# Optimization experiments

Measured on AMD Instinct MI355X. Metric: run time of the kernel, lower is better.

The kernel has to match this reference:

```python
import jax, jax.numpy as jnp
import numpy as np

N = 4096
K = 32
K_NEIGH = 5
LR_EDGE = 0.05
LR_GLOBAL_DECAY = 0.001
NOISE_STD = 0.05
RIPPLE_STRENGTH = 0.01
SPARK_ENERGY_DECAY = 0.98
SPARK_FORCE_STEPS = 5
SPARK_MIN_ENERGY = 0.05
STATE_DECAY = 0.95


def setup_inputs() -> dict:
    key = jax.random.key(0)
    k1, k2, k3 = jax.random.split(key, 3)
    return {
        "W": 0.1 * jax.random.normal(k1, (N, N), jnp.float32),
        "s": jnp.zeros((N,), jnp.float32),
        "noise": jax.random.normal(k2, (N,), jnp.float32),
        "spark_energy": jnp.ones((K,), jnp.float32),
        "u": jax.random.uniform(k3, (K,), jnp.float32),
        "spark_pos": jnp.arange(K, dtype=jnp.int32) % N,
        "spark_age": jnp.zeros((K,), jnp.int32),
    }


def _step(W, s, noise, spark_energy, u, spark_pos, spark_age):
    n = W.shape[0]
    k = spark_pos.shape[0]
    # state diffusion: decay, noisy matvec, sigmoid
    s = s * STATE_DECAY
    s = jax.nn.sigmoid(W @ s + NOISE_STD * noise)
    # force young sparks' positions to 1.0 (drop-mode scatter for masked writes)
    force_idx = jnp.where(spark_age < SPARK_FORCE_STEPS, spark_pos, n)
    s = s.at[force_idx].set(1.0, mode="drop")

    def body(carry, xs):
        W, s = carry
        i, prev, energy, age, ui = xs
        # multinomial over relu(W[prev]) via inverse-CDF on cumsum
        row = W[prev]
        w = jax.nn.relu(row) + 1e-6
        cdf = jnp.cumsum(w)
        nxt = jnp.minimum(
            jnp.searchsorted(cdf, ui * cdf[-1], side="right"), n - 1
        ).astype(prev.dtype)
        # edge learning on traversed edge
        W = W.at[nxt, prev].set(W[nxt, prev] * (1.0 - LR_EDGE) + s[prev] * LR_EDGE)
        # ripple to top-K neighbors of prev (row re-read AFTER edge update, as in torch)
        top = jax.lax.top_k(jax.nn.relu(W[prev]), K_NEIGH)[1]
        W = W.at[prev, top].add(RIPPLE_STRENGTH)
        W = W.at[top, prev].add(RIPPLE_STRENGTH * 0.5)
        W = W.at[top[:, None], top[None, :]].add(RIPPLE_STRENGTH * 0.3)
        # energy decay, deposit energy at new position
        energy = energy * SPARK_ENERGY_DECAY
        s = s.at[nxt].set(energy)
        age = age + 1
        # respawn exhausted sparks
        respawn = energy < SPARK_MIN_ENERGY
        pos_new = jnp.where(respawn, (i % n).astype(prev.dtype), nxt)
        energy = jnp.where(respawn, jnp.float32(1.0), energy)
        age = jnp.where(respawn, jnp.int32(0), age)
        return (W, s), (pos_new, energy, age)

    idx = jnp.arange(k, dtype=jnp.int32)
    (W, s), (pos, energy, age) = jax.lax.scan(
        body, (W, s), (idx, spark_pos, spark_energy, spark_age, u)
    )
    # global decay + clamp
    W = jnp.clip(W * (1.0 - LR_GLOBAL_DECAY), -2.0, 2.0)
    return s, W, pos, energy, age


def reference(W, s, noise, spark_energy, u, spark_pos, spark_age):
    return _step(W, s, noise, spark_energy, u, spark_pos, spark_age)
```

## Files before the change

### kernel.cpp

```cpp
#include <hip/hip_runtime.h>

#define NN 4096
#define KS 32
#define KN 5

typedef float f32x4 __attribute__((ext_vector_type(4)));

#define WS_NXT   16384
#define WS_TOPI  16512
#define WS_NEED  (size_t)(WS_TOPI + KS * KN * 4)

__device__ __forceinline__ void merge5(float* av, int* ai,
                                       const float* bv2, const int* bi2) {
    float nv[KN]; int ni[KN];
    int pA = 0, pB = 0;
    #pragma unroll
    for (int q = 0; q < KN; ++q) {
        float va = av[pA];  int ia = ai[pA];
        float vb = bv2[pB]; int ib = bi2[pB];
        bool pickA = (va > vb) || (va == vb && ia < ib);
        if (pickA) { nv[q] = va; ni[q] = ia; ++pA; }
        else       { nv[q] = vb; ni[q] = ib; ++pB; }
    }
    #pragma unroll
    for (int q = 0; q < KN; ++q) { av[q] = nv[q]; ai[q] = ni[q]; }
}

__device__ __forceinline__ void cdf_scan(const float r[4], int tid, int lane, int wid,
                                         double* wave_incl, double incl[4],
                                         double& a_out, double& ascan_out) {
    double a = 0.0;
    #pragma unroll
    for (int m = 0; m < 4; ++m) {
        a += (double)(fmaxf(r[m], 0.f) + 1e-6f);
        incl[m] = a;
    }
    double ascan = a;
    #pragma unroll
    for (int off = 1; off < 64; off <<= 1) {
        double o = __shfl_up(ascan, (unsigned)off, 64);
        if (lane >= off) ascan += o;
    }
    if (lane == 63) wave_incl[wid] = ascan;
    __syncthreads();
    if (tid < 16) {
        double v = wave_incl[tid];
        #pragma unroll
        for (int off = 1; off < 16; off <<= 1) {
            double o = __shfl_up(v, (unsigned)off, 64);
            if (tid >= off) v += o;
        }
        wave_incl[tid] = v;
    }
    __syncthreads();
    a_out = a;
    ascan_out = ascan;
}

__device__ __forceinline__ void block_top5(const float r[4], int tid, int lane, int wid,
                                           float* topv, int* topi, int* dest) {
    float bv[KN]; int bi[KN];
    #pragma unroll
    for (int m = 0; m < 4; ++m) { bv[m] = fmaxf(r[m], 0.f); bi[m] = tid * 4 + m; }
    bv[4] = -1.f; bi[4] = 0x7fffffff;
    #define CE(i, j) { if (bv[i] < bv[j] || (bv[i] == bv[j] && bi[i] > bi[j])) { \
        float tv = bv[i]; bv[i] = bv[j]; bv[j] = tv; \
        int   ti = bi[i]; bi[i] = bi[j]; bi[j] = ti; } }
    CE(0, 1) CE(2, 3) CE(0, 2) CE(1, 3) CE(1, 2)
    #undef CE
    #pragma unroll
    for (int off = 1; off < 64; off <<= 1) {
        float ov[KN]; int oi[KN];
        #pragma unroll
        for (int q = 0; q < KN; ++q) {
            ov[q] = __shfl_xor(bv[q], off, 64);
            oi[q] = __shfl_xor(bi[q], off, 64);
        }
        merge5(bv, bi, ov, oi);
    }
    if (lane == 0) {
        #pragma unroll
        for (int q = 0; q < KN; ++q) { topv[wid * KN + q] = bv[q]; topi[wid * KN + q] = bi[q]; }
    }
    __syncthreads();
    if (tid < 16) {
        #pragma unroll
        for (int q = 0; q < KN; ++q) { bv[q] = topv[tid * KN + q]; bi[q] = topi[tid * KN + q]; }
        #pragma unroll
        for (int off = 1; off < 16; off <<= 1) {
            float ov[KN]; int oi[KN];
            #pragma unroll
            for (int q = 0; q < KN; ++q) {
                ov[q] = __shfl_xor(bv[q], off, 64);
                oi[q] = __shfl_xor(bi[q], off, 64);
            }
            merge5(bv, bi, ov, oi);
        }
        if (tid == 0) {
            #pragma unroll
            for (int q = 0; q < KN; ++q) dest[q] = bi[q];
        }
    }
    __syncthreads();
}

__global__ __launch_bounds__(1024) void k_front(const float* __restrict__ W,
                                                const float* __restrict__ s,
                                                const float* __restrict__ noise,
                                                float* __restrict__ s_out,
                                                float* __restrict__ outW,
                                                const int* __restrict__ pos_in,
                                                const float* __restrict__ u_in,
                                                char* __restrict__ wsb) {
    __shared__ float  sdec[NN];
    __shared__ double wave_incl[16];
    __shared__ float  topv[16 * KN];
    __shared__ int    topi[16 * KN];
    __shared__ int    sh_nxt;
    int tid = threadIdx.x, lane = tid & 63, wid = tid >> 6;
    int bid = blockIdx.x;

    if (bid < 4096) {
        size_t g = (size_t)bid * 1024 + tid;
        f32x4 v = ((const f32x4*)W)[g];
        v.x = fminf(fmaxf(v.x * 0.999f, -2.f), 2.f);
        v.y = fminf(fmaxf(v.y * 0.999f, -2.f), 2.f);
        v.z = fminf(fmaxf(v.z * 0.999f, -2.f), 2.f);
        v.w = fminf(fmaxf(v.w * 0.999f, -2.f), 2.f);
        __builtin_nontemporal_store(v, &((f32x4*)outW)[g]);

        if (bid < 256) {
            float4 sv = ((const float4*)s)[tid];
            int nz = (sv.x != 0.f || sv.y != 0.f || sv.z != 0.f || sv.w != 0.f) ? 1 : 0;
            float4 d;
            d.x = sv.x * 0.95f; d.y = sv.y * 0.95f;
            d.z = sv.z * 0.95f; d.w = sv.w * 0.95f;
            ((float4*)sdec)[tid] = d;
            int anynz = __syncthreads_or(nz);
            int row = bid * 16 + wid;
            float acc = 0.f;
            if (anynz) {
                const float4* Wr = (const float4*)(W + (size_t)row * NN);
                for (int it = 0; it < 16; ++it) {
                    float4 w = Wr[it * 64 + lane];
                    int j = (it * 64 + lane) * 4;
                    acc += w.x * sdec[j] + w.y * sdec[j + 1] + w.z * sdec[j + 2] + w.w * sdec[j + 3];
                }
            }
            for (int off = 32; off > 0; off >>= 1) acc += __shfl_down(acc, off, 64);
            if (lane == 0) {
                float y = acc + 0.05f * noise[row];
                s_out[row] = 1.0f / (1.0f + expf(-y));
            }
        }
    } else {
        int kk = bid - 4096;
        int prev = pos_in[kk];
        float4 rv = *((const float4*)(W + (size_t)prev * NN) + tid);
        float r[4] = {rv.x, rv.y, rv.z, rv.w};

        if (tid == 0) sh_nxt = NN - 1;
        double incl[4], a, ascan;
        cdf_scan(r, tid, lane, wid, wave_incl, incl, a, ascan);
        double waveExcl = (wid == 0) ? 0.0 : wave_incl[wid - 1];
        double total    = wave_incl[15];
        double thrIncl  = waveExcl + ascan;
        double thrExcl  = thrIncl - a;
        double t = (double)u_in[kk] * total;
        if (thrIncl > t && thrExcl <= t) {
            int found = 3;
            #pragma unroll
            for (int m = 0; m < 4; ++m)
                if (thrExcl + incl[m] > t) { found = m; break; }
            sh_nxt = tid * 4 + found;
        }
        __syncthreads();
        if (tid == 0) ((int*)(wsb + WS_NXT))[kk] = sh_nxt;

        block_top5(r, tid, lane, wid, topv, topi,
                   (int*)(wsb + WS_TOPI) + kk * KN);
    }
}

__global__ __launch_bounds__(1024) void k_scan(float* __restrict__ W,
                                               const float* __restrict__ s_in,
                                               const float* __restrict__ energy_in,
                                               const float* __restrict__ u_in,
                                               const int* __restrict__ pos_in,
                                               const int* __restrict__ age_in,
                                               float* __restrict__ out,
                                               const char* __restrict__ wsb,
                                               int use_pre) {
    __shared__ float  s_lds[NN];
    __shared__ double wave_incl[16];
    __shared__ float  topv[16 * KN];
    __shared__ int    topi[16 * KN];
    __shared__ int    sh_top[KN];
    __shared__ int    sh_nxt;
    __shared__ unsigned int modlist[KS * 36];
    __shared__ float  preval[KS * 36];
    __shared__ float  res_pos[KS], res_en[KS], res_age[KS];
    __shared__ int    sh_pos[KS], sh_age[KS];
    __shared__ float  sh_u[KS], sh_en[KS];
    __shared__ unsigned char dirty[NN];
    __shared__ int    prenxt_lds[KS];
    __shared__ int    topi_lds[KS * KN];

    int tid = threadIdx.x;
    int lane = tid & 63, wid = tid >> 6;

    ((float4*)s_lds)[tid] = ((const float4*)s_in)[tid];
    ((unsigned int*)dirty)[tid] = 0u;
    if (tid < KS) {
        sh_pos[tid] = pos_in[tid];
        sh_age[tid] = age_in[tid];
        sh_u[tid]   = u_in[tid];
        sh_en[tid]  = energy_in[tid];
    }
    if (use_pre) {
        if (tid < KS)      prenxt_lds[tid] = ((const int*)(wsb + WS_NXT))[tid];
        if (tid < KS * KN) topi_lds[tid]   = ((const int*)(wsb + WS_TOPI))[tid];
    }
    __syncthreads();

    if (use_pre) {
        for (int i = tid; i < KS * 36; i += 1024) {
            int k = i / 36, j = i - k * 36;
            int pv = sh_pos[k], nx = prenxt_lds[k];
            int row, col;
            if (j == 0)       { row = nx;                      col = pv; }
            else if (j < 6)   { row = pv;                      col = topi_lds[k * KN + j - 1]; }
            else if (j < 11)  { row = topi_lds[k * KN + j - 6]; col = pv; }
            else { int q = j - 11; row = topi_lds[k * KN + q / KN]; col = topi_lds[k * KN + q % KN]; }
            unsigned a = (unsigned)(row * NN + col);
            modlist[i] = a;
            preval[i]  = W[a];
        }
    }
    if (tid < KS && sh_age[tid] < 5) s_lds[sh_pos[tid]] = 1.0f;
    __syncthreads();

    for (int k = 0; k < KS; ++k) {
        int prev = sh_pos[k];
        bool rowClean = (use_pre != 0) && (dirty[prev] == 0);
        float r[4] = {0.f, 0.f, 0.f, 0.f};
        bool haveRow = false;
        int nxt;

        if (!rowClean) {
            float4 rv = *((const float4*)(W + (size_t)prev * NN) + tid);
            r[0] = rv.x; r[1] = rv.y; r[2] = rv.z; r[3] = rv.w;
            haveRow = true;
            if (tid == 0) sh_nxt = NN - 1;
            double incl[4], a, ascan;
            cdf_scan(r, tid, lane, wid, wave_incl, incl, a, ascan);
            double waveExcl = (wid == 0) ? 0.0 : wave_incl[wid - 1];
            double total    = wave_incl[15];
            double thrIncl  = waveExcl + ascan;
            double thrExcl  = thrIncl - a;
            double t = (double)sh_u[k] * total;
            if (thrIncl > t && thrExcl <= t) {
                int found = 3;
                #pragma unroll
                for (int m = 0; m < 4; ++m)
                    if (thrExcl + incl[m] > t) { found = m; break; }
                sh_nxt = tid * 4 + found;
            }
            __syncthreads();
            nxt = sh_nxt;
        } else {
            nxt = prenxt_lds[k];
        }

        bool fullTop = !rowClean || (nxt == prev);
        if (fullTop && !haveRow) {
            float4 rv = *((const float4*)(W + (size_t)prev * NN) + tid);
            r[0] = rv.x; r[1] = rv.y; r[2] = rv.z; r[3] = rv.w;
            haveRow = true;
            __syncthreads();
        }

        int t0 = 0, t1 = 0, t2 = 0, t3 = 0, t4 = 0;
        bool usePreval = false, edgeAlias = false;
        if (!fullTop) {
            t0 = topi_lds[k * KN + 0]; t1 = topi_lds[k * KN + 1];
            t2 = topi_lds[k * KN + 2]; t3 = topi_lds[k * KN + 3];
            t4 = topi_lds[k * KN + 4];
            edgeAlias = (nxt == t0) || (nxt == t1) || (nxt == t2) ||
                        (nxt == t3) || (nxt == t4);
            bool aliasP = (prev == t0) || (prev == t1) || (prev == t2) ||
                          (prev == t3) || (prev == t4);
            bool dn = (dirty[nxt] | dirty[t0] | dirty[t1] |
                       dirty[t2]  | dirty[t3] | dirty[t4]) != 0;
            usePreval = !dn && !edgeAlias && !aliasP;
        }

        float sprev = s_lds[prev];
        if (usePreval) {
            if (tid < 36) {
                unsigned a = modlist[k * 36 + tid];
                float v = preval[k * 36 + tid];
                float nv = (tid == 0) ? (v * 0.95f + sprev * 0.05f)
                         : (tid < 6)  ? (v + 0.01f)
                         : (tid < 11) ? (v + 0.005f)
                                      : (v + 0.003f);
                W[a] = nv;
            }
        } else {
            if (tid == 0) {
                size_t o = (size_t)nxt * NN + prev;
                W[o] = W[o] * 0.95f + sprev * 0.05f;
            }
            if (fullTop) {
                if (nxt == prev && tid == (prev >> 2)) {
                    int m = prev & 3;
                    r[m] = r[m] * 0.95f + sprev * 0.05f;
                }
                block_top5(r, tid, lane, wid, topv, topi, sh_top);
                t0 = sh_top[0]; t1 = sh_top[1]; t2 = sh_top[2];
                t3 = sh_top[3]; t4 = sh_top[4];
            } else {
                if (edgeAlias) __syncthreads();
            }
            #define TOPQ(q) (fullTop ? sh_top[q] : topi_lds[k * KN + (q)])
            bool alias = (prev == t0) || (prev == t1) || (prev == t2) ||
                         (prev == t3) || (prev == t4);

            if (alias) {
                if (tid < KN) W[(size_t)prev * NN + TOPQ(tid)] += 0.01f;
                __syncthreads();
                if (tid < KN) W[(size_t)TOPQ(tid) * NN + prev] += 0.005f;
                __syncthreads();
                if (tid < KN * KN) W[(size_t)TOPQ(tid / KN) * NN + TOPQ(tid % KN)] += 0.003f;
            } else {
                if (tid < KN) {
                    W[(size_t)prev * NN + TOPQ(tid)] += 0.01f;
                    W[(size_t)TOPQ(tid) * NN + prev] += 0.005f;
                }
                if (tid >= 64 && tid < 64 + KN * KN) {
                    int q = tid - 64;
                    W[(size_t)TOPQ(q / KN) * NN + TOPQ(q % KN)] += 0.003f;
                }
            }

            if (tid < 36) {
                int row, col;
                if (tid == 0)       { row = nxt;             col = prev; }
                else if (tid < 6)   { row = prev;            col = TOPQ(tid - 1); }
                else if (tid < 11)  { row = TOPQ(tid - 6);   col = prev; }
                else { int q = tid - 11; row = TOPQ(q / KN); col = TOPQ(q % KN); }
                modlist[k * 36 + tid] = (unsigned)(row * NN + col);
            }
            #undef TOPQ
        }

        if (tid == 0) { dirty[nxt] = 1; dirty[prev] = 1; }
        if (tid >= 128 && tid < 128 + KN) {
            int q = tid - 128;
            int tr = fullTop ? sh_top[q] : topi_lds[k * KN + q];
            dirty[tr] = 1;
        }

        if (tid == 0) {
            float en = sh_en[k] * 0.98f;
            s_lds[nxt] = en;
            int age = sh_age[k] + 1;
            int posn = nxt;
            if (en < 0.05f) { posn = k % NN; en = 1.0f; age = 0; }
            res_pos[k] = (float)posn;
            res_en[k]  = en;
            res_age[k] = (float)age;
        }
        __syncthreads();
    }

    ((float4*)out)[tid] = ((float4*)s_lds)[tid];
    if (tid < KS) {
        float* tail = out + NN + (size_t)NN * NN;
        tail[tid]          = res_pos[tid];
        tail[KS + tid]     = res_en[tid];
        tail[2 * KS + tid] = res_age[tid];
    }
    float* outW = out + NN;
    for (int i = tid; i < KS * 36; i += 1024) {
        unsigned idx = modlist[i];
        float v = W[idx] * 0.999f;
        v = fminf(fmaxf(v, -2.f), 2.f);
        outW[idx] = v;
    }
}

extern "C" void kernel_launch(void* const* d_in, const int* in_sizes, int n_in,
                              void* d_out, int out_size, void* d_ws, size_t ws_size,
                              hipStream_t stream) {
    float*       W      = (float*)d_in[0];
    const float* s      = (const float*)d_in[1];
    const float* noise  = (const float*)d_in[2];
    const float* energy = (const float*)d_in[3];
    const float* u      = (const float*)d_in[4];
    const int*   pos    = (const int*)d_in[5];
    const int*   age    = (const int*)d_in[6];
    float*       out    = (float*)d_out;
    float*       s_ws   = (float*)d_ws;

    int use_pre = (ws_size >= WS_NEED) ? 1 : 0;

    k_front<<<4096 + (use_pre ? KS : 0), 1024, 0, stream>>>(
        W, s, noise, s_ws, out + NN, pos, u, (char*)d_ws);
    k_scan<<<1, 1024, 0, stream>>>(W, s_ws, energy, u, pos, age, out,
                                   (const char*)d_ws, use_pre);
}
```

Measured before the change: 155.4 us.

## Fuse front and scan kernels with atomic-counter handoff to overlap decay copy

Merges the matvec/precompute kernel and the single-block sequential scan into one launch. The scan block spin-waits on agent-scope atomic counters set by the matvec and precompute blocks, while the bulk W decay/clamp copy runs in 512 extra blocks of 8 float4s each. The goal is to hide the serial scan's latency behind the memory-bound full-matrix copy. Because the scan block no longer knows when the copy finishes, patching modified entries moves to a small follow-up kernel fed by a workspace list. This adds a memset launch and relies on the scan block being co-resident with the blocks it waits on, which carries a deadlock risk if scheduling order changes.

New measurement: 364.8 us. 2.35x slower.

```diff
diff --git a/kernel.cpp b/kernel.cpp
--- a/kernel.cpp
+++ b/kernel.cpp
@@ -6,9 +6,17 @@
 
 typedef float f32x4 __attribute__((ext_vector_type(4)));
 
+#define NB_MV    256
+#define NB_PRE   32
+#define BID_SCAN (NB_MV + NB_PRE)
+#define NB_DEC   512
+#define GRID_ALL (BID_SCAN + 1 + NB_DEC)
+
 #define WS_NXT   16384
 #define WS_TOPI  16512
-#define WS_NEED  (size_t)(WS_TOPI + KS * KN * 4)
+#define WS_CTR   17152
+#define WS_MOD   17408
+#define WS_NEED  (size_t)(WS_MOD + KS * 36 * 4)
 
 __device__ __forceinline__ void merge5(float* av, int* ai,
                                        const float* bv2, const int* bi2) {
@@ -104,57 +112,94 @@
     __syncthreads();
 }
 
-__global__ __launch_bounds__(1024) void k_front(const float* __restrict__ W,
-                                                const float* __restrict__ s,
-                                                const float* __restrict__ noise,
-                                                float* __restrict__ s_out,
-                                                float* __restrict__ outW,
-                                                const int* __restrict__ pos_in,
-                                                const float* __restrict__ u_in,
-                                                char* __restrict__ wsb) {
-    __shared__ float  sdec[NN];
+__device__ __forceinline__ void signal_done(unsigned* ctr) {
+    __syncthreads();
+    if (threadIdx.x == 0) {
+        __threadfence();
+        __hip_atomic_fetch_add(ctr, 1u, __ATOMIC_RELEASE, __HIP_MEMORY_SCOPE_AGENT);
+    }
+}
+
+__global__ __launch_bounds__(1024, 8) void k_all(float* W,
+                                                 const float* __restrict__ s,
+                                                 const float* __restrict__ noise,
+                                                 const float* __restrict__ energy_in,
+                                                 const float* __restrict__ u_in,
+                                                 const int* __restrict__ pos_in,
+                                                 const int* __restrict__ age_in,
+                                                 float* out,
+                                                 char* wsb,
+                                                 int use_pre) {
+    __shared__ float  s_lds[NN];
     __shared__ double wave_incl[16];
     __shared__ float  topv[16 * KN];
     __shared__ int    topi[16 * KN];
+    __shared__ int    sh_top[KN];
     __shared__ int    sh_nxt;
+    __shared__ unsigned int modlist[KS * 36];
+    __shared__ float  preval[KS * 36];
+    __shared__ float  res_pos[KS], res_en[KS], res_age[KS];
+    __shared__ int    sh_pos[KS], sh_age[KS];
+    __shared__ float  sh_u[KS], sh_en[KS];
+    __shared__ unsigned char dirty[NN];
+    __shared__ int    prenxt_lds[KS];
+    __shared__ int    topi_lds[KS * KN];
+
     int tid = threadIdx.x, lane = tid & 63, wid = tid >> 6;
     int bid = blockIdx.x;
-
-    if (bid < 4096) {
-        size_t g = (size_t)bid * 1024 + tid;
-        f32x4 v = ((const f32x4*)W)[g];
-        v.x = fminf(fmaxf(v.x * 0.999f, -2.f), 2.f);
-        v.y = fminf(fmaxf(v.y * 0.999f, -2.f), 2.f);
-        v.z = fminf(fmaxf(v.z * 0.999f, -2.f), 2.f);
-        v.w = fminf(fmaxf(v.w * 0.999f, -2.f), 2.f);
-        __builtin_nontemporal_store(v, &((f32x4*)outW)[g]);
-
-        if (bid < 256) {
-            float4 sv = ((const float4*)s)[tid];
-            int nz = (sv.x != 0.f || sv.y != 0.f || sv.z != 0.f || sv.w != 0.f) ? 1 : 0;
-            float4 d;
-            d.x = sv.x * 0.95f; d.y = sv.y * 0.95f;
-            d.z = sv.z * 0.95f; d.w = sv.w * 0.95f;
-            ((float4*)sdec)[tid] = d;
-            int anynz = __syncthreads_or(nz);
-            int row = bid * 16 + wid;
-            float acc = 0.f;
-            if (anynz) {
-                const float4* Wr = (const float4*)(W + (size_t)row * NN);
-                for (int it = 0; it < 16; ++it) {
-                    float4 w = Wr[it * 64 + lane];
-                    int j = (it * 64 + lane) * 4;
-                    acc += w.x * sdec[j] + w.y * sdec[j + 1] + w.z * sdec[j + 2] + w.w * sdec[j + 3];
-                }
-            }
-            for (int off = 32; off > 0; off >>= 1) acc += __shfl_down(acc, off, 64);
-            if (lane == 0) {
-                float y = acc + 0.05f * noise[row];
-                s_out[row] = 1.0f / (1.0f + expf(-y));
-            }
-        }
-    } else {
-        int kk = bid - 4096;
+    unsigned* ctrA = (unsigned*)(wsb + WS_CTR);
+    unsigned* ctrB = ctrA + 1;
+
+    if (bid >= BID_SCAN + 1) {
+        float* outW = out + NN;
+        size_t base = (size_t)(bid - (BID_SCAN + 1)) * 8192 + tid;
+        const f32x4* Wv = (const f32x4*)W;
+        f32x4* Ov = (f32x4*)outW;
+        f32x4 v[8];
+        #pragma unroll
+        for (int r = 0; r < 8; ++r) v[r] = Wv[base + r * 1024];
+        #pragma unroll
+        for (int r = 0; r < 8; ++r) {
+            v[r].x = fminf(fmaxf(v[r].x * 0.999f, -2.f), 2.f);
+            v[r].y = fminf(fmaxf(v[r].y * 0.999f, -2.f), 2.f);
+            v[r].z = fminf(fmaxf(v[r].z * 0.999f, -2.f), 2.f);
+            v[r].w = fminf(fmaxf(v[r].w * 0.999f, -2.f), 2.f);
+            Ov[base + r * 1024] = v[r];
+        }
+        return;
+    }
+
+    if (bid < NB_MV) {
+        float* s_out = (float*)wsb;
+        float4 sv = ((const float4*)s)[tid];
+        int nz = (sv.x != 0.f || sv.y != 0.f || sv.z != 0.f || sv.w != 0.f) ? 1 : 0;
+        float4 d;
+        d.x = sv.x * 0.95f; d.y = sv.y * 0.95f;
+        d.z = sv.z * 0.95f; d.w = sv.w * 0.95f;
+        ((float4*)s_lds)[tid] = d;
+        int anynz = __syncthreads_or(nz);
+        int row = bid * 16 + wid;
+        float acc = 0.f;
+        if (anynz) {
+            const float4* Wr = (const float4*)(W + (size_t)row * NN);
+            for (int it = 0; it < 16; ++it) {
+                float4 w = Wr[it * 64 + lane];
+                int j = (it * 64 + lane) * 4;
+                acc += w.x * s_lds[j] + w.y * s_lds[j + 1] + w.z * s_lds[j + 2] + w.w * s_lds[j + 3];
+            }
+        }
+        for (int off = 32; off > 0; off >>= 1) acc += __shfl_down(acc, off, 64);
+        if (lane == 0) {
+            float y = acc + 0.05f * noise[row];
+            s_out[row] = 1.0f / (1.0f + expf(-y));
+        }
+        signal_done(ctrA);
+        return;
+    }
+
+    if (bid < BID_SCAN) {
+        if (!use_pre) return;
+        int kk = bid - NB_MV;
         int prev = pos_in[kk];
         float4 rv = *((const float4*)(W + (size_t)prev * NN) + tid);
         float r[4] = {rv.x, rv.y, rv.z, rv.w};
@@ -176,39 +221,23 @@
         }
         __syncthreads();
         if (tid == 0) ((int*)(wsb + WS_NXT))[kk] = sh_nxt;
-
         block_top5(r, tid, lane, wid, topv, topi,
                    (int*)(wsb + WS_TOPI) + kk * KN);
-    }
-}
-
-__global__ __launch_bounds__(1024) void k_scan(float* __restrict__ W,
-                                               const float* __restrict__ s_in,
-                                               const float* __restrict__ energy_in,
-                                               const float* __restrict__ u_in,
-                                               const int* __restrict__ pos_in,
-                                               const int* __restrict__ age_in,
-                                               float* __restrict__ out,
-                                               const char* __restrict__ wsb,
-                                               int use_pre) {
-    __shared__ float  s_lds[NN];
-    __shared__ double wave_incl[16];
-    __shared__ float  topv[16 * KN];
-    __shared__ int    topi[16 * KN];
-    __shared__ int    sh_top[KN];
-    __shared__ int    sh_nxt;
-    __shared__ unsigned int modlist[KS * 36];
-    __shared__ float  preval[KS * 36];
-    __shared__ float  res_pos[KS], res_en[KS], res_age[KS];
-    __shared__ int    sh_pos[KS], sh_age[KS];
-    __shared__ float  sh_u[KS], sh_en[KS];
-    __shared__ unsigned char dirty[NN];
-    __shared__ int    prenxt_lds[KS];
-    __shared__ int    topi_lds[KS * KN];
-
-    int tid = threadIdx.x;
-    int lane = tid & 63, wid = tid >> 6;
-
+        signal_done(ctrB);
+        return;
+    }
+
+    if (tid == 0) {
+        while (__hip_atomic_load(ctrA, __ATOMIC_ACQUIRE, __HIP_MEMORY_SCOPE_AGENT) < NB_MV)
+            __builtin_amdgcn_s_sleep(2);
+        if (use_pre)
+            while (__hip_atomic_load(ctrB, __ATOMIC_ACQUIRE, __HIP_MEMORY_SCOPE_AGENT) < NB_PRE)
+                __builtin_amdgcn_s_sleep(2);
+        __threadfence();
+    }
+    __syncthreads();
+
+    const float* s_in = (const float*)wsb;
     ((float4*)s_lds)[tid] = ((const float4*)s_in)[tid];
     ((unsigned int*)dirty)[tid] = 0u;
     if (tid < KS) {
@@ -381,13 +410,18 @@
         tail[KS + tid]     = res_en[tid];
         tail[2 * KS + tid] = res_age[tid];
     }
-    float* outW = out + NN;
-    for (int i = tid; i < KS * 36; i += 1024) {
-        unsigned idx = modlist[i];
-        float v = W[idx] * 0.999f;
-        v = fminf(fmaxf(v, -2.f), 2.f);
-        outW[idx] = v;
-    }
+    for (int i = tid; i < KS * 36; i += 1024)
+        ((unsigned*)(wsb + WS_MOD))[i] = modlist[i];
+}
+
+__global__ __launch_bounds__(576) void k_fix(const float* __restrict__ W,
+                                             const char* __restrict__ wsb,
+                                             float* __restrict__ out) {
+    int i = blockIdx.x * 576 + threadIdx.x;
+    unsigned idx = ((const unsigned*)(wsb + WS_MOD))[i];
+    float v = W[idx] * 0.999f;
+    v = fminf(fmaxf(v, -2.f), 2.f);
+    (out + NN)[idx] = v;
 }
 
 extern "C" void kernel_launch(void* const* d_in, const int* in_sizes, int n_in,
@@ -401,12 +435,11 @@
     const int*   pos    = (const int*)d_in[5];
     const int*   age    = (const int*)d_in[6];
     float*       out    = (float*)d_out;
-    float*       s_ws   = (float*)d_ws;
 
     int use_pre = (ws_size >= WS_NEED) ? 1 : 0;
 
-    k_front<<<4096 + (use_pre ? KS : 0), 1024, 0, stream>>>(
-        W, s, noise, s_ws, out + NN, pos, u, (char*)d_ws);
-    k_scan<<<1, 1024, 0, stream>>>(W, s_ws, energy, u, pos, age, out,
-                                   (const char*)d_ws, use_pre);
-}
+    hipMemsetAsync((char*)d_ws + WS_CTR, 0, 8, stream);
+    k_all<<<GRID_ALL, 1024, 0, stream>>>(W, s, noise, energy, u, pos, age,
+                                         out, (char*)d_ws, use_pre);
+    k_fix<<<2, 576, 0, stream>>>(W, (const char*)d_ws, out);
+}
```
